# Kernel tuning notes

Hardware: AMD Instinct MI355X
Metric: run time of the kernel (lower is better)

The kernel has to match this reference:

```python
import jax, jax.numpy as jnp
import numpy as np
from jax import lax

NB_DIGITS = 2
BASE = 10
NUMS = BASE ** NB_DIGITS            # 100 possible values per number
SUMS = 2 * (NUMS - 1) + 1           # 199 possible sums (circuit roots)
B = 4096                            # logical batch size
N_IMAGES = B * 2 * NB_DIGITS        # 16384 digit images


def setup_inputs() -> dict:
    key = jax.random.key(0)
    ks = jax.random.split(key, 11)
    s = 0.1
    return {
        "images": jax.random.normal(ks[0], (N_IMAGES, 1, 28, 28), jnp.float32),
        "conv1_w": jax.random.normal(ks[1], (6, 1, 5, 5), jnp.float32) * s,
        "conv1_b": jax.random.normal(ks[2], (6,), jnp.float32) * s,
        "conv2_w": jax.random.normal(ks[3], (16, 6, 5, 5), jnp.float32) * s,
        "conv2_b": jax.random.normal(ks[4], (16,), jnp.float32) * s,
        "fc1_w": jax.random.normal(ks[5], (120, 256), jnp.float32) * s,
        "fc1_b": jax.random.normal(ks[6], (120,), jnp.float32) * s,
        "fc2_w": jax.random.normal(ks[7], (84, 120), jnp.float32) * s,
        "fc2_b": jax.random.normal(ks[8], (84,), jnp.float32) * s,
        "fc3_w": jax.random.normal(ks[9], (10, 84), jnp.float32) * s,
        "fc3_b": jax.random.normal(ks[10], (10,), jnp.float32) * s,
    }


def _conv(x, w, b):
    y = lax.conv_general_dilated(x, w, (1, 1), 'VALID',
                                 dimension_numbers=('NCHW', 'OIHW', 'NCHW'))
    return y + b[None, :, None, None]


def _maxpool2(x):
    return lax.reduce_window(x, -jnp.inf, lax.max, (1, 1, 2, 2), (1, 1, 2, 2), 'VALID')


def _lenet(x, c1w, c1b, c2w, c2b, f1w, f1b, f2w, f2b, f3w, f3b):
    x = jax.nn.relu(_maxpool2(_conv(x, c1w, c1b)))   # [N,6,12,12]
    x = jax.nn.relu(_maxpool2(_conv(x, c2w, c2b)))   # [N,16,4,4]
    x = x.reshape(-1, 16 * 4 * 4)
    x = jax.nn.relu(x @ f1w.T + f1b)
    x = jax.nn.relu(x @ f2w.T + f2b)
    x = x @ f3w.T + f3b
    return jax.nn.log_softmax(x, axis=-1)            # [N,10]


def _circuit(lp):
    # lp: [B, 2*NB_DIGITS, 10] per-digit log-probs.
    # Vars layout from get_circuit: positions 0..NB_DIGITS-1 = n1 digits (MSB first),
    # positions NB_DIGITS..2*NB_DIGITS-1 = n2 digits. Neg-literal weights are 0 in
    # log space (the `zeros` arg), so each model's weight = sum of digit log-probs;
    # OR over models = logsumexp grouped by n1+n2.
    d = jnp.arange(NUMS)
    hi, lo = d // BASE, d % BASE
    lp1 = lp[:, 0, hi] + lp[:, 1, lo]                # [B, NUMS] log P(n1=k)
    lp2 = lp[:, 2, hi] + lp[:, 3, lo]                # [B, NUMS] log P(n2=k)
    M = (lp1[:, :, None] + lp2[:, None, :]).reshape(lp.shape[0], -1)  # [B, NUMS^2]
    seg = (jnp.arange(NUMS)[:, None] + jnp.arange(NUMS)[None, :]).reshape(-1)
    Mf = M.T                                          # [NUMS^2, B]
    m = jax.ops.segment_max(Mf, seg, num_segments=SUMS)              # [SUMS, B]
    ssum = jax.ops.segment_sum(jnp.exp(Mf - m[seg]), seg, num_segments=SUMS)
    return (jnp.log(ssum) + m).T                      # [B, SUMS] log P(sum=s)


def reference(images, conv1_w, conv1_b, conv2_w, conv2_b,
              fc1_w, fc1_b, fc2_w, fc2_b, fc3_w, fc3_b):
    logp = _lenet(images, conv1_w, conv1_b, conv2_w, conv2_b,
                  fc1_w, fc1_b, fc2_w, fc2_b, fc3_w, fc3_b)   # [N_IMAGES,10]
    lp = logp.reshape(B, 2 * NB_DIGITS, BASE)
    return _circuit(lp)
```

## Files before the change

### kernel.cpp

```cpp
#include <hip/hip_runtime.h>
#include <hip/hip_bf16.h>
#include <math.h>

#define SUMS 199
#define NBLK 1024

typedef __attribute__((ext_vector_type(8))) short short8;
typedef __attribute__((ext_vector_type(4))) float float4v;

union Frag8 { short8 v; unsigned u[4]; uint4 q; };

static __device__ inline unsigned pk_bf16(float a, float b) {
    __hip_bfloat162 h = __float22bfloat162_rn(make_float2(a, b));
    union { __hip_bfloat162 h; unsigned u; } c; c.h = h; return c.u;
}

__global__ __launch_bounds__(256) void convert_weights(
    const float* __restrict__ f1w, const float* __restrict__ f2w,
    const float* __restrict__ f3w, const float* __restrict__ c1w,
    const float* __restrict__ c2w, uint4* __restrict__ ws)
{
    const int g = blockIdx.x * 256 + threadIdx.x;
    if (g >= 6400) return;
    float v[8];
    if (g < 5824) {
        const float* W; int O, K, ld, nt, s, l;
        if (g < 4096)      { W = f1w; O = 120; K = 256; ld = 256; nt = g >> 9; s = (g >> 6) & 7; l = g & 63; }
        else if (g < 5632) { const int f = g - 4096; W = f2w; O = 84; K = 120; ld = 120; nt = f >> 8; s = (f >> 6) & 3; l = f & 63; }
        else               { const int f = g - 5632; W = f3w; O = 10; K = 84;  ld = 84;  nt = 0; s = f >> 6; l = f & 63; }
        const int o = nt * 16 + (l & 15);
        #pragma unroll
        for (int j = 0; j < 8; ++j) {
            const int k = 32 * s + 8 * (l >> 4) + j;
            v[j] = (o < O && k < K) ? W[o * ld + k] : 0.f;
        }
    } else if (g < 6336) {
        const int f = g - 5824, s = f >> 6, l = f & 63;
        const int c = l & 15, h = l >> 4;
        #pragma unroll
        for (int jp = 0; jp < 4; ++jp) {
            const int D = 16 * s + 4 * h + jp;
            const int ky = D / 24, rem = D % 24, kx = rem >> 2, icp = rem & 3;
            const bool ok = (ky < 5 && kx < 5);
            v[2 * jp]     = (ok && 2 * icp < 6)     ? c2w[c * 150 + (2 * icp) * 25 + ky * 5 + kx]     : 0.f;
            v[2 * jp + 1] = (ok && 2 * icp + 1 < 6) ? c2w[c * 150 + (2 * icp + 1) * 25 + ky * 5 + kx] : 0.f;
        }
    } else {
        const int l = (g - 6336) & 63;
        const int c = l & 15, h = l >> 4;
        const int oc = c >> 1, xs = c & 1;
        #pragma unroll
        for (int j = 0; j < 8; ++j) {
            const int p = h * 4 + (j >> 1);
            float w = 0.f;
            if (p < 15 && c < 12) {
                const int ky = p / 3, kx = 2 * (p % 3) + (j & 1) - xs;
                if (kx >= 0 && kx < 5) w = c1w[oc * 25 + ky * 5 + kx];
            }
            v[j] = w;
        }
    }
    uint4 r;
    r.x = pk_bf16(v[0], v[1]); r.y = pk_bf16(v[2], v[3]);
    r.z = pk_bf16(v[4], v[5]); r.w = pk_bf16(v[6], v[7]);
    ws[g] = r;
}

__global__ __launch_bounds__(256) void lenet_circuit_kernel(
    const float* __restrict__ images,
    const float* __restrict__ c1b, const float* __restrict__ c2b,
    const float* __restrict__ f1b, const float* __restrict__ f2b,
    const float* __restrict__ f3b, const uint4* __restrict__ wsb,
    float* __restrict__ out)
{
    __shared__ __align__(16) unsigned char s_mem[39712];
    unsigned*       imgu = (unsigned*)s_mem;
    unsigned short* p1s  = (unsigned short*)(s_mem + 12576);
    const uint4*    p1u4 = (const uint4*)(s_mem + 12576);
    unsigned*       A1d  = (unsigned*)(s_mem + 31264);
    const uint4*    A1q  = (const uint4*)(s_mem + 31264);
    float*          E1Pf = (float*)(s_mem + 12576);
    float*          E2Rf = (float*)(s_mem + 19232);

    const int t = threadIdx.x, bid = blockIdx.x;
    const int lane = t & 63, wav = t >> 6;
    const int c = lane & 15, h = lane >> 4;
    const uint4 z4 = {0u, 0u, 0u, 0u};

    {
        uint4* pz = (uint4*)(s_mem + 12576);
        for (int i = t; i < 1168; i += 256) pz[i] = z4;
    }
    Frag8 a1; a1.q = wsb[6336 + lane];
    Frag8 w2[8];
    #pragma unroll
    for (int s = 0; s < 8; ++s) w2[s].q = wsb[5824 + s * 64 + lane];
    int koff[8];
    #pragma unroll
    for (int s = 0; s < 8; ++s) {
        const int D0 = 16 * s + 4 * h;
        koff[s] = (D0 / 24) * 12 + ((D0 % 24) >> 2);
    }
    int pd[4];
    #pragma unroll
    for (int q = 0; q < 4; ++q) {
        const int p = 4 * h + q;
        pd[q] = (p < 15) ? (p / 3) * 14 + (p % 3) : 0;
    }
    float bias0 = 0.f, bias1 = 0.f;
    if (h < 3) { bias0 = c1b[2 * h]; bias1 = c1b[2 * h + 1]; }
    const float b2v = c2b[c];

    for (int pass = 0; pass < 2; ++pass) {
        {
            const float4* g = (const float4*)(images + (size_t)bid * 12544 + pass * 6272);
            for (int i = t; i < 1568; i += 256) {
                const float4 v = g[i];
                const int im = i / 196, j = i % 196;
                imgu[im * 393 + 2 * j]     = pk_bf16(v.x, v.y);
                imgu[im * 393 + 2 * j + 1] = pk_bf16(v.z, v.w);
            }
        }
        __syncthreads();

        {
            const int n = c, img = n >> 1;
            const int imb = img * 393 + (n & 1) * 14;
            for (int qy = wav * 3; qy < wav * 3 + 3; ++qy) {
                #pragma unroll
                for (int qx = 0; qx < 12; ++qx) {
                    const int base = imb + qy * 28 + qx;
                    Frag8 bf;
                    #pragma unroll
                    for (int q = 0; q < 4; ++q) bf.u[q] = imgu[base + pd[q]];
                    float4v acc = {0.f, 0.f, 0.f, 0.f};
                    acc = __builtin_amdgcn_mfma_f32_16x16x32_bf16(a1.v, bf.v, acc, 0, 0, 0);
                    float v0 = fmaxf(acc[0], acc[1]);
                    float v1 = fmaxf(acc[2], acc[3]);
                    v0 = fmaxf(v0, __shfl_xor(v0, 1));
                    v1 = fmaxf(v1, __shfl_xor(v1, 1));
                    if ((n & 1) == 0 && h < 3) {
                        const unsigned pkv = pk_bf16(fmaxf(v0 + bias0, 0.f),
                                                     fmaxf(v1 + bias1, 0.f));
                        *(unsigned*)&p1s[img * 1152 + qy * 96 + qx * 8 + 2 * h] = pkv;
                    }
                }
            }
        }
        __syncthreads();

        {
            const int pxl = (c & 1) + 2 * ((c >> 2) & 1);
            const int pyl = ((c >> 1) & 1) + 2 * ((c >> 3) & 1);
            #pragma unroll
            for (int ii = 0; ii < 2; ++ii) {
                const int i0 = 2 * wav + ii;
                #pragma unroll
                for (int mt = 0; mt < 4; ++mt) {
                    const int px = pxl + 4 * (mt & 1), py = pyl + 4 * (mt >> 1);
                    const int base = i0 * 144 + py * 12 + px;
                    float4v acc = {0.f, 0.f, 0.f, 0.f};
                    #pragma unroll
                    for (int s = 0; s < 8; ++s) {
                        Frag8 af; af.q = p1u4[base + koff[s]];
                        acc = __builtin_amdgcn_mfma_f32_16x16x32_bf16(af.v, w2[s].v, acc, 0, 0, 0);
                    }
                    const float p = fmaxf(fmaxf(acc[0], acc[1]), fmaxf(acc[2], acc[3]));
                    float v = fmaxf(p + b2v, 0.f);
                    const float vp = __shfl_xor(v, 16);
                    if ((h & 1) == 0) {
                        const int qy = (h >> 1) + 2 * (mt >> 1);
                        A1d[(pass * 8 + i0) * 132 + c * 8 + qy * 2 + (mt & 1)] = pk_bf16(v, vp);
                    }
                }
            }
        }
    }
    __syncthreads();

    {
        uint4* pz = (uint4*)(s_mem + 12576);
        for (int i = t; i < 832; i += 256) pz[i] = z4;
        unsigned* A2d = (unsigned*)s_mem;
        if (t < 64) A2d[(t >> 2) * 68 + 60 + (t & 3)] = 0u;
        float4v acc0 = {0.f, 0.f, 0.f, 0.f}, acc1 = acc0;
        const int nt0 = 2 * wav;
        #pragma unroll
        for (int s = 0; s < 8; ++s) {
            Frag8 af; af.q = A1q[c * 33 + 4 * s + h];
            Frag8 b0; b0.q = wsb[(nt0 * 8 + s) * 64 + lane];
            Frag8 b1; b1.q = wsb[((nt0 + 1) * 8 + s) * 64 + lane];
            acc0 = __builtin_amdgcn_mfma_f32_16x16x32_bf16(af.v, b0.v, acc0, 0, 0, 0);
            acc1 = __builtin_amdgcn_mfma_f32_16x16x32_bf16(af.v, b1.v, acc1, 0, 0, 0);
        }
        #pragma unroll
        for (int ntl = 0; ntl < 2; ++ntl) {
            const int o = 32 * wav + 16 * ntl + c;
            const float bias = (o < 120) ? f1b[o] : 0.f;
            #pragma unroll
            for (int r = 0; r < 4; ++r) {
                float v = fmaxf((ntl ? acc1[r] : acc0[r]) + bias, 0.f);
                const float vp = __shfl_xor(v, 1);
                if ((c & 1) == 0 && o < 120)
                    A2d[(4 * h + r) * 68 + (o >> 1)] = pk_bf16(v, vp);
            }
        }
    }
    __syncthreads();

    {
        unsigned* A3d = (unsigned*)(s_mem + 4352);
        if (t < 96) A3d[(t / 6) * 52 + 42 + (t % 6)] = 0u;
        if (wav < 3) {
            const uint4* A2q = (const uint4*)s_mem;
            float4v acc0 = {0.f, 0.f, 0.f, 0.f}, acc1 = acc0;
            const int nt0 = 2 * wav;
            #pragma unroll
            for (int s = 0; s < 4; ++s) {
                Frag8 af; af.q = A2q[c * 17 + 4 * s + h];
                Frag8 b0; b0.q = wsb[4096 + (nt0 * 4 + s) * 64 + lane];
                Frag8 b1; b1.q = wsb[4096 + ((nt0 + 1) * 4 + s) * 64 + lane];
                acc0 = __builtin_amdgcn_mfma_f32_16x16x32_bf16(af.v, b0.v, acc0, 0, 0, 0);
                acc1 = __builtin_amdgcn_mfma_f32_16x16x32_bf16(af.v, b1.v, acc1, 0, 0, 0);
            }
            #pragma unroll
            for (int ntl = 0; ntl < 2; ++ntl) {
                const int o = 32 * wav + 16 * ntl + c;
                const float bias = (o < 84) ? f2b[o] : 0.f;
                #pragma unroll
                for (int r = 0; r < 4; ++r) {
                    float v = fmaxf((ntl ? acc1[r] : acc0[r]) + bias, 0.f);
                    const float vp = __shfl_xor(v, 1);
                    if ((c & 1) == 0 && o < 84)
                        A3d[(4 * h + r) * 52 + (o >> 1)] = pk_bf16(v, vp);
                }
            }
        }
    }
    __syncthreads();

    float* lgf = (float*)(s_mem + 7680);

    if (wav == 0) {
        const uint4* A3q = (const uint4*)(s_mem + 4352);
        float4v acc = {0.f, 0.f, 0.f, 0.f};
        #pragma unroll
        for (int s = 0; s < 3; ++s) {
            Frag8 af; af.q = A3q[c * 13 + 4 * s + h];
            Frag8 b; b.q = wsb[5632 + s * 64 + lane];
            acc = __builtin_amdgcn_mfma_f32_16x16x32_bf16(af.v, b.v, acc, 0, 0, 0);
        }
        const float bias = (c < 10) ? f3b[c] : 0.f;
        float x[4], m[4], sm[4];
        #pragma unroll
        for (int r = 0; r < 4; ++r) {
            x[r] = (c < 10) ? (acc[r] + bias) : -INFINITY;
            m[r] = x[r];
        }
        #pragma unroll
        for (int d = 1; d <= 8; d <<= 1)
            #pragma unroll
            for (int r = 0; r < 4; ++r) m[r] = fmaxf(m[r], __shfl_xor(m[r], d));
        #pragma unroll
        for (int r = 0; r < 4; ++r) sm[r] = (c < 10) ? expf(x[r] - m[r]) : 0.f;
        #pragma unroll
        for (int d = 1; d <= 8; d <<= 1)
            #pragma unroll
            for (int r = 0; r < 4; ++r) sm[r] += __shfl_xor(sm[r], d);
        if (c < 10) {
            #pragma unroll
            for (int r = 0; r < 4; ++r)
                lgf[(4 * h + r) * 12 + c] = x[r] - (m[r] + logf(sm[r]));
        }
    }
    __syncthreads();

    for (int idx = t; idx < 800; idx += 256) {
        const int be = idx / 200, r = idx % 200;
        const float* lp = lgf + 4 * be * 12;
        if (r < 100) {
            const float v = expf(lp[r / 10] + lp[12 + r % 10]);
            #pragma unroll
            for (int ph = 0; ph < 4; ++ph)
                E1Pf[(ph * 4 + be) * 104 + r + ph] = v;
        } else {
            const int k = r - 100;
            const float v = expf(lp[24 + k / 10] + lp[36 + k % 10]);
            #pragma unroll
            for (int ph = 0; ph < 4; ++ph)
                E2Rf[(ph * 4 + be) * 104 + (99 - k) + ph] = v;
        }
    }
    __syncthreads();

    for (int pid = t; pid < 400; pid += 256) {
        const int be = pid / 100, sp = pid % 100;
        float* ob = out + ((size_t)bid * 4 + be) * SUMS;
        #pragma unroll
        for (int form = 0; form < 2; ++form) {
            const int o1 = form ? sp : 0;
            const int o2 = form ? 0 : 99 - sp;
            const int len = form ? 100 - sp : sp + 1;
            if (form && sp == 0) break;
            const int ph1 = (4 - (o1 & 3)) & 3, ph2 = (4 - (o2 & 3)) & 3;
            const float4* P1 = (const float4*)(E1Pf + (ph1 * 4 + be) * 104) + ((o1 + ph1) >> 2);
            const float4* P2 = (const float4*)(E2Rf + (ph2 * 4 + be) * 104) + ((o2 + ph2) >> 2);
            const int nv = (len + 3) >> 2;
            float s = 0.f;
            for (int j = 0; j < nv; ++j) {
                const float4 a = P1[j], b = P2[j];
                s += a.x * b.x + a.y * b.y + a.z * b.z + a.w * b.w;
            }
            ob[form ? sp + 99 : sp] = logf(s);
        }
    }
}

extern "C" void kernel_launch(void* const* d_in, const int* in_sizes, int n_in,
                              void* d_out, int out_size, void* d_ws, size_t ws_size,
                              hipStream_t stream) {
    const float* images = (const float*)d_in[0];
    const float* c1w = (const float*)d_in[1];
    const float* c1b = (const float*)d_in[2];
    const float* c2w = (const float*)d_in[3];
    const float* c2b = (const float*)d_in[4];
    const float* f1w = (const float*)d_in[5];
    const float* f1b = (const float*)d_in[6];
    const float* f2w = (const float*)d_in[7];
    const float* f2b = (const float*)d_in[8];
    const float* f3w = (const float*)d_in[9];
    const float* f3b = (const float*)d_in[10];
    float* out = (float*)d_out;

    convert_weights<<<25, 256, 0, stream>>>(f1w, f2w, f3w, c1w, c2w, (uint4*)d_ws);
    lenet_circuit_kernel<<<NBLK, 256, 0, stream>>>(
        images, c1b, c2b, f1b, f2b, f3b, (const uint4*)d_ws, out);
}
```

Before: 146.2 us.

## Factor sum-of-digits circuit into per-digit-place convolutions instead of full 100x100 correlation

Replaces the 100-length correlation of number probabilities with a factorized form: the tens digits are convolved into a 19-entry distribution H and the units digits into a 19-entry L, then each of the 199 sums combines a few H·L terms. This removes the expf over 200 number probabilities, the padded phase-shifted shared buffers, their zeroing and the O(100) dot products per output. It works in probability space (softmax probabilities rather than log-probs), so very small probabilities could underflow where the old code, also working in exp space, behaved similarly.

```diff
diff --git a/kernel.cpp b/kernel.cpp
--- a/kernel.cpp
+++ b/kernel.cpp
@@ -79,8 +79,9 @@
     const uint4*    p1u4 = (const uint4*)(s_mem + 12576);
     unsigned*       A1d  = (unsigned*)(s_mem + 31264);
     const uint4*    A1q  = (const uint4*)(s_mem + 31264);
-    float*          E1Pf = (float*)(s_mem + 12576);
-    float*          E2Rf = (float*)(s_mem + 19232);
+    float*          pgf  = (float*)(s_mem + 7680);
+    float*          Hf   = (float*)(s_mem + 8448);
+    float*          Lf   = (float*)(s_mem + 8768);
 
     const int t = threadIdx.x, bid = blockIdx.x;
     const int lane = t & 63, wav = t >> 6;
@@ -179,8 +180,6 @@
     __syncthreads();
 
     {
-        uint4* pz = (uint4*)(s_mem + 12576);
-        for (int i = t; i < 832; i += 256) pz[i] = z4;
         unsigned* A2d = (unsigned*)s_mem;
         if (t < 64) A2d[(t >> 2) * 68 + 60 + (t & 3)] = 0u;
         float4v acc0 = {0.f, 0.f, 0.f, 0.f}, acc1 = acc0;
@@ -239,8 +238,6 @@
     }
     __syncthreads();
 
-    float* lgf = (float*)(s_mem + 7680);
-
     if (wav == 0) {
         const uint4* A3q = (const uint4*)(s_mem + 4352);
         float4v acc = {0.f, 0.f, 0.f, 0.f};
@@ -251,7 +248,7 @@
             acc = __builtin_amdgcn_mfma_f32_16x16x32_bf16(af.v, b.v, acc, 0, 0, 0);
         }
         const float bias = (c < 10) ? f3b[c] : 0.f;
-        float x[4], m[4], sm[4];
+        float x[4], m[4], e[4], sm[4];
         #pragma unroll
         for (int r = 0; r < 4; ++r) {
             x[r] = (c < 10) ? (acc[r] + bias) : -INFINITY;
@@ -262,7 +259,7 @@
             #pragma unroll
             for (int r = 0; r < 4; ++r) m[r] = fmaxf(m[r], __shfl_xor(m[r], d));
         #pragma unroll
-        for (int r = 0; r < 4; ++r) sm[r] = (c < 10) ? expf(x[r] - m[r]) : 0.f;
+        for (int r = 0; r < 4; ++r) { e[r] = (c < 10) ? expf(x[r] - m[r]) : 0.f; sm[r] = e[r]; }
         #pragma unroll
         for (int d = 1; d <= 8; d <<= 1)
             #pragma unroll
@@ -270,49 +267,34 @@
         if (c < 10) {
             #pragma unroll
             for (int r = 0; r < 4; ++r)
-                lgf[(4 * h + r) * 12 + c] = x[r] - (m[r] + logf(sm[r]));
-        }
-    }
-    __syncthreads();
-
-    for (int idx = t; idx < 800; idx += 256) {
-        const int be = idx / 200, r = idx % 200;
-        const float* lp = lgf + 4 * be * 12;
-        if (r < 100) {
-            const float v = expf(lp[r / 10] + lp[12 + r % 10]);
-            #pragma unroll
-            for (int ph = 0; ph < 4; ++ph)
-                E1Pf[(ph * 4 + be) * 104 + r + ph] = v;
-        } else {
-            const int k = r - 100;
-            const float v = expf(lp[24 + k / 10] + lp[36 + k % 10]);
-            #pragma unroll
-            for (int ph = 0; ph < 4; ++ph)
-                E2Rf[(ph * 4 + be) * 104 + (99 - k) + ph] = v;
-        }
-    }
-    __syncthreads();
-
-    for (int pid = t; pid < 400; pid += 256) {
-        const int be = pid / 100, sp = pid % 100;
-        float* ob = out + ((size_t)bid * 4 + be) * SUMS;
-        #pragma unroll
-        for (int form = 0; form < 2; ++form) {
-            const int o1 = form ? sp : 0;
-            const int o2 = form ? 0 : 99 - sp;
-            const int len = form ? 100 - sp : sp + 1;
-            if (form && sp == 0) break;
-            const int ph1 = (4 - (o1 & 3)) & 3, ph2 = (4 - (o2 & 3)) & 3;
-            const float4* P1 = (const float4*)(E1Pf + (ph1 * 4 + be) * 104) + ((o1 + ph1) >> 2);
-            const float4* P2 = (const float4*)(E2Rf + (ph2 * 4 + be) * 104) + ((o2 + ph2) >> 2);
-            const int nv = (len + 3) >> 2;
-            float s = 0.f;
-            for (int j = 0; j < nv; ++j) {
-                const float4 a = P1[j], b = P2[j];
-                s += a.x * b.x + a.y * b.y + a.z * b.z + a.w * b.w;
-            }
-            ob[form ? sp + 99 : sp] = logf(s);
-        }
+                pgf[(4 * h + r) * 12 + c] = e[r] / sm[r];
+        }
+    }
+    __syncthreads();
+
+    if (t < 152) {
+        const int be = t / 38, j = t % 38;
+        const int isH = (j < 19), b = isH ? j : j - 19;
+        const float* pg = pgf + 4 * be * 12;
+        const float* PA = pg + (isH ? 0 : 12);
+        const float* PB = pg + (isH ? 24 : 36);
+        const int ilo = (b > 9) ? b - 9 : 0;
+        const int ihi = (b < 9) ? b : 9;
+        float s = 0.f;
+        for (int i = ilo; i <= ihi; ++i) s += PA[i] * PB[b - i];
+        (isH ? Hf : Lf)[be * 20 + b] = s;
+    }
+    __syncthreads();
+
+    for (int idx = t; idx < 4 * SUMS; idx += 256) {
+        const int be = idx / SUMS, s = idx % SUMS;
+        const float* H = Hf + be * 20;
+        const float* L = Lf + be * 20;
+        const int bmin = (s > 18) ? (s - 9) / 10 : 0;
+        int bmax = s / 10; if (bmax > 18) bmax = 18;
+        float sum = 0.f;
+        for (int b = bmin; b <= bmax; ++b) sum += H[b] * L[s - 10 * b];
+        out[((size_t)bid * 4 + be) * SUMS + s] = logf(sum);
     }
 }
 
```

After: 139.6 us. -4.5%, faster.
